# Kernel tuning notes

Measured on AMD Instinct MI355X. Metric: run time of the kernel, lower is better.

## Reference

```python
import jax, jax.numpy as jnp
import numpy as np

B, L, T = 64, 256, 800
NMEL, PRE, ARNN, DRNN, ENC, ATT, NF, K = 80, 256, 512, 512, 512, 128, 32, 31
ZP = 0.1  # zoneout prob (eval-mode expected-value interpolation)


def setup_inputs() -> dict:
    key = jax.random.key(0)
    ks = iter(jax.random.split(key, 32))
    def p(shape, s=0.05):
        return jax.random.normal(next(ks), shape, dtype=jnp.float32) * s
    inp = {
        'encoder_out': jax.random.normal(next(ks), (B, L, ENC), dtype=jnp.float32),
        'lengths': jax.random.randint(next(ks), (B,), L // 2, L + 1),
        'mels': jax.random.normal(next(ks), (B, T, NMEL), dtype=jnp.float32),
        # prenet: 3 bias-free linears with relu (eval: dropout off)
        'Wp1': p((PRE, NMEL)), 'Wp2': p((PRE, PRE)), 'Wp3': p((PRE, PRE)),
        # attention LSTMCell: input = prenet_dim + enc = 768
        'aWih': p((4 * ARNN, PRE + ENC)), 'aWhh': p((4 * ARNN, ARNN)),
        'abih': jnp.zeros((4 * ARNN,)), 'abhh': jnp.zeros((4 * ARNN,)),
        # decoder LSTMCell: input = att_rnn + enc = 1024
        'dWih': p((4 * DRNN, ARNN + ENC)), 'dWhh': p((4 * DRNN, DRNN)),
        'dbih': jnp.zeros((4 * DRNN,)), 'dbhh': jnp.zeros((4 * DRNN,)),
        # location-sensitive attention (all bias-free)
        'Wq': p((ATT, ARNN)), 'Wm': p((ATT, ENC)),
        'Wconv': p((NF, 2, K)), 'Wloc': p((ATT, NF)), 'v': p((1, ATT)),
        # output projection + gate
        'Wout': p((NMEL, DRNN + ENC)), 'bout': jnp.zeros((NMEL,)),
        'Wgate': p((1, DRNN + ENC)), 'bgate': jnp.zeros((1,)),
    }
    return inp


def _lstm(x, h, c, Wih, Whh, bih, bhh):
    g = x @ Wih.T + h @ Whh.T + (bih + bhh)
    i, f, gg, o = jnp.split(g, 4, axis=-1)
    c2 = jax.nn.sigmoid(f) * c + jax.nn.sigmoid(i) * jnp.tanh(gg)
    return jax.nn.sigmoid(o) * jnp.tanh(c2), c2


def _zoneout(new, old):
    return ZP * old + (1.0 - ZP) * new


def decoder_forward(encoder_out, lengths, mels, Wp1, Wp2, Wp3,
                    aWih, aWhh, abih, abhh, dWih, dWhh, dbih, dbhh,
                    Wq, Wm, Wconv, Wloc, v, Wout, bout, Wgate, bgate):
    b, l, _ = encoder_out.shape
    t = mels.shape[1]
    processed_memory = encoder_out @ Wm.T                       # (B,L,ATT)
    mask = jnp.arange(l)[None, :] >= lengths[:, None]           # True = padded
    # teacher forcing inputs: shift mels right by one zero frame
    dec_in = jnp.concatenate(
        [jnp.zeros((b, 1, NMEL), encoder_out.dtype), mels[:, :t - 1]], axis=1)
    xs = jnp.swapaxes(dec_in, 0, 1)                             # (T,B,NMEL)

    def step(carry, frame):
        ah, ac, dh, dc, ctx, aw, aws = carry
        x = jax.nn.relu(jax.nn.relu(jax.nn.relu(frame @ Wp1.T) @ Wp2.T) @ Wp3.T)
        ah2, ac2 = _lstm(jnp.concatenate([x, ctx], -1), ah, ac, aWih, aWhh, abih, abhh)
        ah2, ac2 = _zoneout(ah2, ah), _zoneout(ac2, ac)
        # location features: conv over (B,2,L)
        aw_cat = jnp.stack([aw, aws], axis=1)
        loc = jax.lax.conv_general_dilated(
            aw_cat, Wconv, window_strides=(1,), padding=[((K - 1) // 2,) * 2],
            dimension_numbers=('NCH', 'OIH', 'NCH'))                # (B,NF,L)
        ploc = jnp.swapaxes(loc, 1, 2) @ Wloc.T                      # (B,L,ATT)
        e = jnp.tanh(ah2[:, None, :] @ Wq.T + processed_memory + ploc)
        energies = jnp.squeeze(e @ v.T, -1)                          # (B,L)
        energies = jnp.where(mask, jnp.float32(-1e9), energies)
        w = jax.nn.softmax(energies, axis=-1)
        ctx2 = jnp.einsum('bl,ble->be', w, encoder_out)
        aws2 = aws + w
        dh2, dc2 = _lstm(jnp.concatenate([ah2, ctx2], -1), dh, dc, dWih, dWhh, dbih, dbhh)
        dh2, dc2 = _zoneout(dh2, dh), _zoneout(dc2, dc)
        dhc = jnp.concatenate([dh2, ctx2], axis=-1)
        mel = dhc @ Wout.T + bout
        gate = jnp.squeeze(dhc @ Wgate.T + bgate, -1)
        return (ah2, ac2, dh2, dc2, ctx2, w, aws2), (mel, gate, w)

    z = lambda *s: jnp.zeros(s, encoder_out.dtype)
    carry0 = (z(b, ARNN), z(b, ARNN), z(b, DRNN), z(b, DRNN), z(b, ENC), z(b, l), z(b, l))
    _, (mel_t, gate_t, align_t) = jax.lax.scan(step, carry0, xs)
    return (jnp.swapaxes(mel_t, 0, 1),      # (B,T,NMEL)
            jnp.swapaxes(gate_t, 0, 1),     # (B,T)
            jnp.swapaxes(align_t, 0, 1))    # (B,T,L)


def reference(encoder_out, lengths, mels, Wp1, Wp2, Wp3,
              aWih, aWhh, abih, abhh, dWih, dWhh, dbih, dbhh,
              Wq, Wm, Wconv, Wloc, v, Wout, bout, Wgate, bgate):
    return decoder_forward(encoder_out, lengths, mels, Wp1, Wp2, Wp3,
                           aWih, aWhh, abih, abhh, dWih, dWhh, dbih, dbhh,
                           Wq, Wm, Wconv, Wloc, v, Wout, bout, Wgate, bgate)
```

## Files before the change

kernel.cpp:

```cpp
#include <hip/hip_runtime.h>


#define DEV_INLINE __device__ __forceinline__

constexpr int TB = 800;

constexpr size_t PMT_O  = 0;
constexpr size_t WQT_O  = 2228224;
constexpr size_t LOCF_O = 2293760;
constexpr size_t Y1_O   = 2818048;
constexpr size_t Y2_O   = 2834432;
constexpr size_t XR_O   = 2850816;
constexpr size_t AH_O   = 2883584;
constexpr size_t AC_O   = 2949120;
constexpr size_t DH_O   = 3014656;
constexpr size_t DC_O   = 3080192;
constexpr size_t CTX_O  = 3145728;
constexpr size_t AW_O   = 3211264;
constexpr size_t AWS_O  = 3244032;
constexpr size_t BAR_O  = 3276800;
constexpr size_t ZERO_N = 991232;

constexpr size_t MEL_O  = 0;
constexpr size_t GATE_O = 4096000;
constexpr size_t ALG_O  = 4147200;

DEV_INLINE float sigf(float x)     { return 1.0f / (1.0f + __expf(-x)); }
DEV_INLINE float tanhfast(float x) { float e = __expf(2.0f * x); return 1.0f - 2.0f / (e + 1.0f); }

DEV_INLINE void stc(float* p, float v) {
  __hip_atomic_store(p, v, __ATOMIC_RELAXED, __HIP_MEMORY_SCOPE_AGENT);
}

struct Params {
  const float* enc; const int* len; const float* mels;
  const float* Wp1; const float* Wp2; const float* Wp3;
  const float* aWih; const float* aWhh; const float* abih; const float* abhh;
  const float* dWih; const float* dWhh; const float* dbih; const float* dbhh;
  const float* Wconv; const float* Wloc; const float* v;
  const float* Wout; const float* bout; const float* Wgate; const float* bgate;
  float* ws; float* out;
};

DEV_INLINE void gbar(unsigned* bar, int blk, bool iscap, unsigned e)
{
  __syncthreads();
  if (threadIdx.x == 0) {
    const unsigned g = (unsigned)blk >> 5;
    unsigned a = __hip_atomic_fetch_add(bar + g * 64, 1u, __ATOMIC_RELAXED, __HIP_MEMORY_SCOPE_AGENT);
    if (a == e * 32u - 1u)
      __hip_atomic_fetch_add(bar + 512, 1u, __ATOMIC_RELAXED, __HIP_MEMORY_SCOPE_AGENT);
    if (iscap) {
      while (__hip_atomic_load(bar + 512, __ATOMIC_RELAXED, __HIP_MEMORY_SCOPE_AGENT) < e * 8u)
        __builtin_amdgcn_s_sleep(1);
      __builtin_amdgcn_fence(__ATOMIC_ACQUIRE, "agent");
      const unsigned nc = __hip_atomic_load(bar + 2176, __ATOMIC_RELAXED, __HIP_MEMORY_SCOPE_AGENT);
      unsigned c = __hip_atomic_fetch_add(bar + 576, 1u, __ATOMIC_RELAXED, __HIP_MEMORY_SCOPE_AGENT);
      if (c == e * nc - 1u) {
#pragma unroll
        for (unsigned i = 0; i < 8; ++i)
          __hip_atomic_store(bar + 640 + i * 64, e, __ATOMIC_RELAXED, __HIP_MEMORY_SCOPE_AGENT);
      }
    }
    {
      const unsigned g2 = (unsigned)blk >> 5;
      while (__hip_atomic_load(bar + 640 + g2 * 64, __ATOMIC_RELAXED, __HIP_MEMORY_SCOPE_AGENT) < e)
        __builtin_amdgcn_s_sleep(4);
    }
  }
  __syncthreads();
  asm volatile("buffer_inv sc0\n\ts_waitcnt vmcnt(0)" ::: "memory");
}

DEV_INLINE void gseg16(float* __restrict__ acc,
                       const float* __restrict__ inT,
                       const float* __restrict__ W, const int ldw, const int wcol0,
                       const int u0, const int segk0, const int seglen,
                       const int ks, const int ke, const int lane)
{
  const int a0 = ks > segk0 ? ks : segk0;
  const int a1 = (ke < segk0 + seglen) ? ke : (segk0 + seglen);
  if (a0 >= a1) return;
  const float* __restrict__ ip = inT + (size_t)(a0 - segk0) * 64 + lane;
  const int n = a1 - a0;
  const float* wp[16];
#pragma unroll
  for (int j = 0; j < 16; ++j) {
    const int row = u0 + (j >> 2) + 512 * (j & 3);
    wp[j] = W + (size_t)row * ldw + (wcol0 + (a0 - segk0));
  }
  for (int k = 0; k < n; k += 4) {
    const float x0 = ip[(k + 0) * 64];
    const float x1 = ip[(k + 1) * 64];
    const float x2 = ip[(k + 2) * 64];
    const float x3 = ip[(k + 3) * 64];
#pragma unroll
    for (int j = 0; j < 16; ++j)
      acc[j] += x0 * wp[j][k] + x1 * wp[j][k + 1] + x2 * wp[j][k + 2] + x3 * wp[j][k + 3];
  }
}

template<int NO>
DEV_INLINE void gseg(float* __restrict__ acc,
                     const float* __restrict__ inT,
                     const float* __restrict__ W, const int ldw, const int wcol0,
                     const int* __restrict__ rows, const int segk0, const int seglen,
                     const int ks, const int ke, const int lane)
{
  const int a0 = ks > segk0 ? ks : segk0;
  const int a1 = (ke < segk0 + seglen) ? ke : (segk0 + seglen);
  if (a0 >= a1) return;
  const float* __restrict__ ip = inT + (size_t)(a0 - segk0) * 64 + lane;
  const int n = a1 - a0;
  const float* wp[NO];
#pragma unroll
  for (int j = 0; j < NO; ++j)
    wp[j] = W + (size_t)rows[j] * ldw + (wcol0 + (a0 - segk0));
  for (int k = 0; k < n; k += 4) {
    const float x0 = ip[(k + 0) * 64];
    const float x1 = ip[(k + 1) * 64];
    const float x2 = ip[(k + 2) * 64];
    const float x3 = ip[(k + 3) * 64];
#pragma unroll
    for (int j = 0; j < NO; ++j)
      acc[j] += x0 * wp[j][k] + x1 * wp[j][k + 1] + x2 * wp[j][k + 2] + x3 * wp[j][k + 3];
  }
}

__global__ __launch_bounds__(256) void init_kernel(const float* __restrict__ Wq,
                                                   float* __restrict__ ws)
{
  const int i = blockIdx.x * 256 + threadIdx.x;
  {
    const int k = i >> 7, a = i & 127;
    ws[WQT_O + i] = Wq[a * 512 + k];
  }
  for (size_t idx = i; idx < ZERO_N; idx += 65536)
    ws[LOCF_O + idx] = 0.0f;
}

__global__ __launch_bounds__(256) void prenet_kernel(const float* __restrict__ mels,
                                                     const float* __restrict__ Wp1,
                                                     const float* __restrict__ Wp2,
                                                     const float* __restrict__ Wp3,
                                                     float* __restrict__ xb)
{
  __shared__ float smem[16384];
  const int t = blockIdx.x;
  const int tid = threadIdx.x;
  const int lane = tid & 63;
  const int wv = __builtin_amdgcn_readfirstlane(tid >> 6);

  if (t == 0) {
    for (int i = tid; i < 5200; i += 256) smem[i] = 0.0f;
  } else {
    for (int i = tid; i < 5120; i += 256) {
      const int b = i / 80, k = i - b * 80;
      smem[k * 65 + b] = mels[((size_t)b * TB + (t - 1)) * 80 + k];
    }
  }
  __syncthreads();

  float va[8][8];
#pragma unroll
  for (int g = 0; g < 8; ++g) {
    const int u0 = wv * 64 + g * 8;
    float acc[8] = {};
    for (int k = 0; k < 80; ++k) {
      const float x = smem[k * 65 + lane];
#pragma unroll
      for (int j = 0; j < 8; ++j) acc[j] += x * Wp1[(u0 + j) * 80 + k];
    }
#pragma unroll
    for (int j = 0; j < 8; ++j) va[g][j] = fmaxf(acc[j], 0.0f);
  }
  __syncthreads();
#pragma unroll
  for (int g = 0; g < 8; ++g)
#pragma unroll
    for (int j = 0; j < 8; ++j) smem[(wv * 64 + g * 8 + j) * 64 + lane] = va[g][j];
  __syncthreads();

#pragma unroll
  for (int g = 0; g < 8; ++g) {
    const int u0 = wv * 64 + g * 8;
    float acc[8] = {};
    for (int k = 0; k < 256; ++k) {
      const float x = smem[k * 64 + lane];
#pragma unroll
      for (int j = 0; j < 8; ++j) acc[j] += x * Wp2[(u0 + j) * 256 + k];
    }
#pragma unroll
    for (int j = 0; j < 8; ++j) va[g][j] = fmaxf(acc[j], 0.0f);
  }
  __syncthreads();
#pragma unroll
  for (int g = 0; g < 8; ++g)
#pragma unroll
    for (int j = 0; j < 8; ++j) smem[(wv * 64 + g * 8 + j) * 64 + lane] = va[g][j];
  __syncthreads();

#pragma unroll
  for (int g = 0; g < 8; ++g) {
    const int u0 = wv * 64 + g * 8;
    float acc[8] = {};
    for (int k = 0; k < 256; ++k) {
      const float x = smem[k * 64 + lane];
#pragma unroll
      for (int j = 0; j < 8; ++j) acc[j] += x * Wp3[(u0 + j) * 256 + k];
    }
#pragma unroll
    for (int j = 0; j < 8; ++j)
      xb[((size_t)t * 256 + (u0 + j)) * 64 + lane] = fmaxf(acc[j], 0.0f);
  }
}

__global__ __launch_bounds__(256) void pm_kernel(const float* __restrict__ enc,
                                                 const float* __restrict__ Wm,
                                                 float* __restrict__ pmT)
{
  __shared__ float encL[64 * 129];
  const int b = blockIdx.x >> 2;
  const int l0 = (blockIdx.x & 3) * 64;
  const int tid = threadIdx.x;
  const int lane = tid & 63;
  const int wv = __builtin_amdgcn_readfirstlane(tid >> 6);

  float acc[4][8];
#pragma unroll
  for (int ai = 0; ai < 4; ++ai)
#pragma unroll
    for (int j = 0; j < 8; ++j) acc[ai][j] = 0.0f;

  for (int kc = 0; kc < 4; ++kc) {
    __syncthreads();
    for (int i = tid; i < 64 * 128; i += 256) {
      const int l = i >> 7, k = i & 127;
      encL[l * 129 + k] = enc[((size_t)b * 256 + l0 + l) * 512 + kc * 128 + k];
    }
    __syncthreads();
#pragma unroll
    for (int ai = 0; ai < 4; ++ai) {
      const int agrp = (ai * 4 + wv) * 8;
      for (int k = 0; k < 128; ++k) {
        const float x = encL[lane * 129 + k];
#pragma unroll
        for (int j = 0; j < 8; ++j)
          acc[ai][j] += x * Wm[(size_t)(agrp + j) * 512 + kc * 128 + k];
      }
    }
  }
#pragma unroll
  for (int ai = 0; ai < 4; ++ai) {
    const int agrp = (ai * 4 + wv) * 8;
#pragma unroll
    for (int j = 0; j < 8; ++j)
      pmT[((size_t)b * 128 + agrp + j) * 256 + l0 + lane] = acc[ai][j];
  }
}


DEV_INLINE void f_dgates4(int u0, int tid, int lane, int wv,
                          const float* __restrict__ ah, const float* __restrict__ dh,
                          float* __restrict__ gdL, const Params& p, float* sm)
{
  float acc[16] = {};
  const int ks = wv * 256, ke = ks + 256;
  gseg16(acc, ah, p.dWih, 1024, 0, u0, 0,   512, ks, ke, lane);
  gseg16(acc, dh, p.dWhh, 512,  0, u0, 512, 512, ks, ke, lane);
#pragma unroll
  for (int j = 0; j < 16; ++j) sm[(wv * 16 + j) * 64 + lane] = acc[j];
  __syncthreads();
  {
    const int m = tid & 63, uq = tid >> 6;
    const int u = u0 + uq;
#pragma unroll
    for (int q = 0; q < 4; ++q) {
      const int j = uq * 4 + q;
      gdL[j * 64 + m] = sm[j * 64 + m] + sm[(16 + j) * 64 + m] + sm[(32 + j) * 64 + m] + sm[(48 + j) * 64 + m]
                      + p.dbih[u + 512 * q] + p.dbhh[u + 512 * q];
    }
  }
  __syncthreads();
}

DEV_INLINE void f_dfin4(int u0, int tid, int lane, int wv,
                        const float* __restrict__ ctx, const float* __restrict__ gdL,
                        float* __restrict__ dh_o, float* __restrict__ dhL, float* __restrict__ dcL,
                        const Params& p, float* sm)
{
  float acc[16] = {};
  const int ks = wv * 128, ke = ks + 128;
  gseg16(acc, ctx, p.dWih, 1024, 512, u0, 0, 512, ks, ke, lane);
#pragma unroll
  for (int j = 0; j < 16; ++j) sm[(wv * 16 + j) * 64 + lane] = acc[j];
  __syncthreads();
  {
    const int m = tid & 63, uq = tid >> 6;
    const int u = u0 + uq;
    float g[4];
#pragma unroll
    for (int q = 0; q < 4; ++q) {
      const int j = uq * 4 + q;
      g[q] = sm[j * 64 + m] + sm[(16 + j) * 64 + m] + sm[(32 + j) * 64 + m] + sm[(48 + j) * 64 + m]
           + gdL[j * 64 + m];
    }
    const float ho = dhL[uq * 64 + m], co = dcL[uq * 64 + m];
    const float c2 = sigf(g[1]) * co + sigf(g[0]) * tanhfast(g[2]);
    const float h2 = sigf(g[3]) * tanhfast(c2);
    const float hn = 0.1f * ho + 0.9f * h2;
    const float cn = 0.1f * co + 0.9f * c2;
    stc(dh_o + (size_t)u * 64 + m, hn);
    dhL[uq * 64 + m] = hn;
    dcL[uq * 64 + m] = cn;
  }
  __syncthreads();
}

DEV_INLINE void f_alstm4(int u0, int tid, int lane, int wv,
                         const float* __restrict__ xt, const float* __restrict__ ctx,
                         const float* __restrict__ ahg,
                         float* __restrict__ ah_o, float* __restrict__ ahL, float* __restrict__ acL,
                         const Params& p, float* sm)
{
  float acc[16] = {};
  const int ks = wv * 320, ke = ks + 320;
  gseg16(acc, xt,  p.aWih, 768, 0,   u0, 0,   256, ks, ke, lane);
  gseg16(acc, ctx, p.aWih, 768, 256, u0, 256, 512, ks, ke, lane);
  gseg16(acc, ahg, p.aWhh, 512, 0,   u0, 768, 512, ks, ke, lane);
#pragma unroll
  for (int j = 0; j < 16; ++j) sm[(wv * 16 + j) * 64 + lane] = acc[j];
  __syncthreads();
  {
    const int m = tid & 63, uq = tid >> 6;
    const int u = u0 + uq;
    float g[4];
#pragma unroll
    for (int q = 0; q < 4; ++q) {
      const int j = uq * 4 + q;
      g[q] = sm[j * 64 + m] + sm[(16 + j) * 64 + m] + sm[(32 + j) * 64 + m] + sm[(48 + j) * 64 + m]
           + p.abih[u + 512 * q] + p.abhh[u + 512 * q];
    }
    const float ho = ahL[uq * 64 + m], co = acL[uq * 64 + m];
    const float c2 = sigf(g[1]) * co + sigf(g[0]) * tanhfast(g[2]);
    const float h2 = sigf(g[3]) * tanhfast(c2);
    const float hn = 0.1f * ho + 0.9f * h2;
    const float cn = 0.1f * co + 0.9f * c2;
    stc(ah_o + (size_t)u * 64 + m, hn);
    ahL[uq * 64 + m] = hn;
    acL[uq * 64 + m] = cn;
  }
  __syncthreads();
}

DEV_INLINE void f_mel(int c0, int tid, int lane, int wv, int tm1,
                      const float* __restrict__ dh, const float* __restrict__ ctx,
                      const Params& p, float* sm)
{
  int rows[4] = {c0, c0 + 1, c0 + 2, c0 + 3};
  float acc[4] = {};
  const int ks = wv * 256, ke = ks + 256;
  gseg<4>(acc, dh,  p.Wout, 1024, 0,   rows, 0,   512, ks, ke, lane);
  gseg<4>(acc, ctx, p.Wout, 1024, 512, rows, 512, 512, ks, ke, lane);
#pragma unroll
  for (int j = 0; j < 4; ++j) sm[(wv * 4 + j) * 64 + lane] = acc[j];
  __syncthreads();
  {
    const int m = tid & 63, c = tid >> 6;
    const float val = sm[c * 64 + m] + sm[(4 + c) * 64 + m] + sm[(8 + c) * 64 + m] + sm[(12 + c) * 64 + m]
                    + p.bout[c0 + c];
    stc(p.out + MEL_O + ((size_t)m * TB + tm1) * 80 + c0 + c, val);
  }
  __syncthreads();
}

DEV_INLINE void f_gate(int tid, int lane, int wv, int tm1,
                       const float* __restrict__ dh, const float* __restrict__ ctx,
                       const Params& p, float* sm)
{
  float acc[1] = {};
  int rows1[1] = {0};
  const int ks = wv * 256, ke = ks + 256;
  gseg<1>(acc, dh,  p.Wgate, 1024, 0,   rows1, 0,   512, ks, ke, lane);
  gseg<1>(acc, ctx, p.Wgate, 1024, 512, rows1, 512, 512, ks, ke, lane);
  sm[wv * 64 + lane] = acc[0];
  __syncthreads();
  if (tid < 64) {
    const float val = sm[tid] + sm[64 + tid] + sm[128 + tid] + sm[192 + tid] + p.bgate[0];
    stc(p.out + GATE_O + (size_t)tid * TB + tm1, val);
  }
  __syncthreads();
}

DEV_INLINE void f_conv(int b, int tid,
                       const float* __restrict__ aw, const float* __restrict__ aws,
                       float* __restrict__ locF, const Params& p, float* sm)
{
  float* awL  = sm;
  float* awsL = sm + 290;
  if (tid < 15) { awL[tid] = 0.0f; awsL[tid] = 0.0f; awL[271 + tid] = 0.0f; awsL[271 + tid] = 0.0f; }
  awL[15 + tid]  = aw[b * 256 + tid];
  awsL[15 + tid] = aws[b * 256 + tid];
  __syncthreads();
  float awv[31], awsv[31];
#pragma unroll
  for (int k = 0; k < 31; ++k) { awv[k] = awL[tid + k]; awsv[k] = awsL[tid + k]; }
  float* dst = locF + ((size_t)b * 256 + tid) * 32;
  for (int f = 0; f < 32; ++f) {
    const float* wc = p.Wconv + f * 62;
    float lf = 0.0f;
#pragma unroll
    for (int k = 0; k < 31; ++k) lf += awv[k] * wc[k] + awsv[k] * wc[31 + k];
    stc(dst + f, lf);
  }
  __syncthreads();
}

DEV_INLINE void f_energy(int b, int t, int tid, int lane, int wv,
                         const float* __restrict__ ah, const float* __restrict__ aws_p,
                         float* __restrict__ ctx_o, float* __restrict__ aw_o,
                         float* __restrict__ aws_o,
                         const float* __restrict__ pmT, const float* __restrict__ wqT,
                         const float* __restrict__ locF, const Params& p, float* sm)
{
  float* ahL = sm;
  float* qpL = sm + 512;
  float* qL  = sm + 768;
  float* red = sm + 896;
  float* wL  = sm + 912;
  ahL[tid]       = ah[(size_t)tid * 64 + b];
  ahL[tid + 256] = ah[(size_t)(tid + 256) * 64 + b];
  __syncthreads();
  {
    const int a = tid & 127, h = tid >> 7;
    float qp = 0.0f;
    const float* wq = wqT + (size_t)(h * 256) * 128 + a;
    const float* xv = ahL + h * 256;
    for (int k = 0; k < 256; k += 4)
      qp += wq[(k + 0) * 128] * xv[k + 0] + wq[(k + 1) * 128] * xv[k + 1]
          + wq[(k + 2) * 128] * xv[k + 2] + wq[(k + 3) * 128] * xv[k + 3];
    qpL[tid] = qp;
  }
  __syncthreads();
  if (tid < 128) qL[tid] = qpL[tid] + qpL[128 + tid];
  __syncthreads();

  float locv[32];
  {
    const float4* lf4 = (const float4*)(locF + ((size_t)b * 256 + tid) * 32);
#pragma unroll
    for (int i = 0; i < 8; ++i) {
      float4 x = lf4[i];
      locv[4*i] = x.x; locv[4*i+1] = x.y; locv[4*i+2] = x.z; locv[4*i+3] = x.w;
    }
  }
  float part = 0.0f;
  const float* pmp = pmT + (size_t)b * 32768 + tid;
#pragma unroll 2
  for (int a = 0; a < 128; ++a) {
    float s = qL[a] + pmp[(size_t)a * 256];
    const float* wl = p.Wloc + a * 32;
#pragma unroll
    for (int f = 0; f < 32; ++f) s += locv[f] * wl[f];
    part += p.v[a] * tanhfast(s);
  }
  if (tid >= p.len[b]) part = -1e9f;

  float mv = part;
  for (int mm = 32; mm >= 1; mm >>= 1) mv = fmaxf(mv, __shfl_xor(mv, mm, 64));
  if (lane == 0) red[wv] = mv;
  __syncthreads();
  const float mx = fmaxf(fmaxf(red[0], red[1]), fmaxf(red[2], red[3]));
  const float pex = __expf(part - mx);
  float ssum = pex;
  for (int mm = 32; mm >= 1; mm >>= 1) ssum += __shfl_xor(ssum, mm, 64);
  if (lane == 0) red[8 + wv] = ssum;
  __syncthreads();
  const float inv = 1.0f / (red[8] + red[9] + red[10] + red[11]);
  const float w = pex * inv;
  wL[tid] = w;
  stc(aw_o + b * 256 + tid, w);
  stc(aws_o + b * 256 + tid, aws_p[b * 256 + tid] + w);
  stc(p.out + ALG_O + ((size_t)b * TB + t) * 256 + tid, w);
  __syncthreads();

  float c0 = 0.0f, c1 = 0.0f;
  const float* ep = p.enc + (size_t)b * 256 * 512;
  for (int l = 0; l < 256; ++l) {
    const float wv_ = wL[l];
    c0 += wv_ * ep[(size_t)l * 512 + tid];
    c1 += wv_ * ep[(size_t)l * 512 + tid + 256];
  }
  stc(ctx_o + (size_t)tid * 64 + b, c0);
  stc(ctx_o + (size_t)(tid + 256) * 64 + b, c1);
  __syncthreads();
}

DEV_INLINE void f_pn1(int blkL, int frame, int lane, int wv,
                      const Params& p, float* __restrict__ y1)
{
  const int u0 = blkL * 32 + wv * 8;
  float acc[8] = {};
  const float* mp = p.mels + ((size_t)lane * TB + frame) * 80;
  for (int k = 0; k < 80; ++k) {
    const float x = mp[k];
#pragma unroll
    for (int j = 0; j < 8; ++j) acc[j] += x * p.Wp1[(u0 + j) * 80 + k];
  }
#pragma unroll
  for (int j = 0; j < 8; ++j) stc(y1 + (size_t)(u0 + j) * 64 + lane, fmaxf(acc[j], 0.0f));
}

DEV_INLINE void f_pnmid(int blkL, int lane, int wv,
                        const float* __restrict__ yin, const float* __restrict__ W,
                        float* __restrict__ yout)
{
  const int u0 = blkL * 32 + wv * 8;
  float acc[8] = {};
  for (int k = 0; k < 256; ++k) {
    const float x = yin[(size_t)k * 64 + lane];
#pragma unroll
    for (int j = 0; j < 8; ++j) acc[j] += x * W[(u0 + j) * 256 + k];
  }
#pragma unroll
  for (int j = 0; j < 8; ++j) stc(yout + (size_t)(u0 + j) * 64 + lane, fmaxf(acc[j], 0.0f));
}

__global__ __launch_bounds__(256) void persist_kernel(Params p)
{
  __shared__ float sm[4096];
  __shared__ float gdL[1024];
  __shared__ float s1L[256];
  __shared__ float s2L[256];
  __shared__ unsigned capflag;

  const int tid = threadIdx.x, blk = blockIdx.x;
  const int lane = tid & 63;
  const int wv = __builtin_amdgcn_readfirstlane(tid >> 6);
  const bool isX = blk < 128;
  const int yi = blk - 128;

  float* ws   = p.ws;
  float* pmT  = ws + PMT_O;
  float* wqT  = ws + WQT_O;
  float* locF = ws + LOCF_O;
  float* y1   = ws + Y1_O;
  float* y2   = ws + Y2_O;
  float* xr   = ws + XR_O;
  float* AH[2]  = {ws + AH_O,  ws + AH_O  + 32768};
  float* DH[2]  = {ws + DH_O,  ws + DH_O  + 32768};
  float* CTX[2] = {ws + CTX_O, ws + CTX_O + 32768};
  float* AW[2]  = {ws + AW_O,  ws + AW_O  + 16384};
  float* AWS[2] = {ws + AWS_O, ws + AWS_O + 16384};
  unsigned* bar = (unsigned*)(ws + BAR_O);

  s1L[tid] = 0.0f; s2L[tid] = 0.0f;
  if (tid == 0) {
    unsigned x;
    asm volatile("s_getreg_b32 %0, hwreg(HW_REG_XCC_ID)" : "=s"(x));
    unsigned prev = __hip_atomic_fetch_add(bar + 2048 + (x & 7), 1u,
                                           __ATOMIC_RELAXED, __HIP_MEMORY_SCOPE_AGENT);
    if (prev == 0)
      __hip_atomic_fetch_add(bar + 2176, 1u, __ATOMIC_RELAXED, __HIP_MEMORY_SCOPE_AGENT);
    capflag = (prev == 0) ? 1u : 0u;
  }
  __syncthreads();
  const bool iscap = (capflag != 0);
  unsigned e = 0;

  if (!isX && yi >= 85 && yi < 93) f_pn1(yi - 85, 1, lane, wv, p, y1);
  gbar(bar, blk, iscap, ++e);

  if (!isX) {
    f_alstm4(yi * 4, tid, lane, wv, xr, CTX[1], AH[1], AH[0], s1L, s2L, p, sm);
  } else if (blk < 8) {
    f_pnmid(blk, lane, wv, y1, p.Wp2, y2);
  }
  gbar(bar, blk, iscap, ++e);

  for (int t = 0; t < TB; ++t) {
    const int cur = t & 1, prv = cur ^ 1;
    if (isX) {
      f_dgates4(blk * 4, tid, lane, wv, AH[cur], DH[prv], gdL, p, sm);
    } else if (yi < 64) {
      f_energy(yi, t, tid, lane, wv, AH[cur], AWS[prv],
               CTX[cur], AW[cur], AWS[cur], pmT, wqT, locF, p, sm);
    } else if (yi < 84) {
      if (t > 0) f_mel((yi - 64) * 4, tid, lane, wv, t - 1, DH[prv], CTX[prv], p, sm);
    } else if (yi == 84) {
      if (t > 0) f_gate(tid, lane, wv, t - 1, DH[prv], CTX[prv], p, sm);
    } else if (yi < 93) {
      if (t <= 796) f_pn1(yi - 85, t + 2, lane, wv, p, y1);
    } else if (yi < 101) {
      if (t <= 797) f_pnmid(yi - 93, lane, wv, y2, p.Wp3, xr + (size_t)cur * 16384);
    }
    gbar(bar, blk, iscap, ++e);

    if (isX) {
      f_dfin4(blk * 4, tid, lane, wv, CTX[cur], gdL, DH[cur], s1L, s2L, p, sm);
      if (blk >= 64) {
        if (t < TB - 1) f_conv(blk - 64, tid, AW[cur], AWS[cur], locF, p, sm);
      } else if (blk < 8) {
        if (t <= 796) f_pnmid(blk, lane, wv, y1, p.Wp2, y2);
      }
    } else {
      if (t < TB - 1)
        f_alstm4(yi * 4, tid, lane, wv, xr + (size_t)prv * 16384, CTX[cur],
                 AH[cur], AH[prv], s1L, s2L, p, sm);
    }
    gbar(bar, blk, iscap, ++e);
  }
  if (!isX) {
    if (yi >= 64 && yi < 84)  f_mel((yi - 64) * 4, tid, lane, wv, TB - 1, DH[1], CTX[1], p, sm);
    else if (yi == 84)        f_gate(tid, lane, wv, TB - 1, DH[1], CTX[1], p, sm);
  }
}

extern "C" void kernel_launch(void* const* d_in, const int* in_sizes, int n_in,
                              void* d_out, int out_size, void* d_ws, size_t ws_size,
                              hipStream_t stream)
{
  (void)in_sizes; (void)n_in; (void)out_size; (void)ws_size;
  Params P;
  P.enc   = (const float*)d_in[0];
  P.len   = (const int*)  d_in[1];
  P.mels  = (const float*)d_in[2];
  P.Wp1   = (const float*)d_in[3];
  P.Wp2   = (const float*)d_in[4];
  P.Wp3   = (const float*)d_in[5];
  P.aWih  = (const float*)d_in[6];
  P.aWhh  = (const float*)d_in[7];
  P.abih  = (const float*)d_in[8];
  P.abhh  = (const float*)d_in[9];
  P.dWih  = (const float*)d_in[10];
  P.dWhh  = (const float*)d_in[11];
  P.dbih  = (const float*)d_in[12];
  P.dbhh  = (const float*)d_in[13];
  const float* Wq = (const float*)d_in[14];
  const float* Wm = (const float*)d_in[15];
  P.Wconv = (const float*)d_in[16];
  P.Wloc  = (const float*)d_in[17];
  P.v     = (const float*)d_in[18];
  P.Wout  = (const float*)d_in[19];
  P.bout  = (const float*)d_in[20];
  P.Wgate = (const float*)d_in[21];
  P.bgate = (const float*)d_in[22];
  P.ws  = (float*)d_ws;
  P.out = (float*)d_out;

  init_kernel<<<256, 256, 0, stream>>>(Wq, P.ws);
  pm_kernel<<<256, 256, 0, stream>>>(P.enc, Wm, P.ws + PMT_O);
  prenet_kernel<<<2, 256, 0, stream>>>(P.mels, P.Wp1, P.Wp2, P.Wp3, P.ws + XR_O);

  persist_kernel<<<256, 256, 0, stream>>>(P);
}
```

Before: 101.8 ms.

## Simplify grid barrier and replace cache invalidation with coherent loads

Replaces the per-XCD captain-based hierarchical barrier with a two-level counter tree whose last arriver releases all group flags. It also drops the full L2/L1 buffer_inv after each barrier. Instead, cross-block activation reads use relaxed agent-scope atomic loads, so weights stay cached. Wloc is staged into LDS for the energy blocks, and the context loop is unrolled. The risk is memory-ordering correctness: there is no acquire fence, and ordering now depends only on relaxed atomics.

```diff
diff --git a/kernel.cpp b/kernel.cpp
--- a/kernel.cpp
+++ b/kernel.cpp
@@ -12,9 +12,7 @@
 constexpr size_t Y2_O   = 2834432;
 constexpr size_t XR_O   = 2850816;
 constexpr size_t AH_O   = 2883584;
-constexpr size_t AC_O   = 2949120;
 constexpr size_t DH_O   = 3014656;
-constexpr size_t DC_O   = 3080192;
 constexpr size_t CTX_O  = 3145728;
 constexpr size_t AW_O   = 3211264;
 constexpr size_t AWS_O  = 3244032;
@@ -30,6 +28,9 @@
 
 DEV_INLINE void stc(float* p, float v) {
   __hip_atomic_store(p, v, __ATOMIC_RELAXED, __HIP_MEMORY_SCOPE_AGENT);
+}
+DEV_INLINE float ldc(const float* p) {
+  return __hip_atomic_load(p, __ATOMIC_RELAXED, __HIP_MEMORY_SCOPE_AGENT);
 }
 
 struct Params {
@@ -42,41 +43,31 @@
   float* ws; float* out;
 };
 
-DEV_INLINE void gbar(unsigned* bar, int blk, bool iscap, unsigned e)
+DEV_INLINE void gbar(unsigned* bar, int blk, unsigned e)
 {
   __syncthreads();
   if (threadIdx.x == 0) {
     const unsigned g = (unsigned)blk >> 5;
     unsigned a = __hip_atomic_fetch_add(bar + g * 64, 1u, __ATOMIC_RELAXED, __HIP_MEMORY_SCOPE_AGENT);
-    if (a == e * 32u - 1u)
-      __hip_atomic_fetch_add(bar + 512, 1u, __ATOMIC_RELAXED, __HIP_MEMORY_SCOPE_AGENT);
-    if (iscap) {
-      while (__hip_atomic_load(bar + 512, __ATOMIC_RELAXED, __HIP_MEMORY_SCOPE_AGENT) < e * 8u)
-        __builtin_amdgcn_s_sleep(1);
-      __builtin_amdgcn_fence(__ATOMIC_ACQUIRE, "agent");
-      const unsigned nc = __hip_atomic_load(bar + 2176, __ATOMIC_RELAXED, __HIP_MEMORY_SCOPE_AGENT);
-      unsigned c = __hip_atomic_fetch_add(bar + 576, 1u, __ATOMIC_RELAXED, __HIP_MEMORY_SCOPE_AGENT);
-      if (c == e * nc - 1u) {
+    if (a == e * 32u - 1u) {
+      unsigned r = __hip_atomic_fetch_add(bar + 512, 1u, __ATOMIC_RELAXED, __HIP_MEMORY_SCOPE_AGENT);
+      if (r == e * 8u - 1u) {
 #pragma unroll
         for (unsigned i = 0; i < 8; ++i)
           __hip_atomic_store(bar + 640 + i * 64, e, __ATOMIC_RELAXED, __HIP_MEMORY_SCOPE_AGENT);
       }
     }
-    {
-      const unsigned g2 = (unsigned)blk >> 5;
-      while (__hip_atomic_load(bar + 640 + g2 * 64, __ATOMIC_RELAXED, __HIP_MEMORY_SCOPE_AGENT) < e)
-        __builtin_amdgcn_s_sleep(4);
-    }
-  }
-  __syncthreads();
-  asm volatile("buffer_inv sc0\n\ts_waitcnt vmcnt(0)" ::: "memory");
-}
-
-DEV_INLINE void gseg16(float* __restrict__ acc,
-                       const float* __restrict__ inT,
-                       const float* __restrict__ W, const int ldw, const int wcol0,
-                       const int u0, const int segk0, const int seglen,
-                       const int ks, const int ke, const int lane)
+    while (__hip_atomic_load(bar + 640 + g * 64, __ATOMIC_RELAXED, __HIP_MEMORY_SCOPE_AGENT) < e)
+      __builtin_amdgcn_s_sleep(2);
+  }
+  __syncthreads();
+}
+
+DEV_INLINE void gseg16C(float* __restrict__ acc,
+                        const float* __restrict__ inT,
+                        const float* __restrict__ W, const int ldw, const int wcol0,
+                        const int u0, const int segk0, const int seglen,
+                        const int ks, const int ke, const int lane)
 {
   const int a0 = ks > segk0 ? ks : segk0;
   const int a1 = (ke < segk0 + seglen) ? ke : (segk0 + seglen);
@@ -90,10 +81,10 @@
     wp[j] = W + (size_t)row * ldw + (wcol0 + (a0 - segk0));
   }
   for (int k = 0; k < n; k += 4) {
-    const float x0 = ip[(k + 0) * 64];
-    const float x1 = ip[(k + 1) * 64];
-    const float x2 = ip[(k + 2) * 64];
-    const float x3 = ip[(k + 3) * 64];
+    const float x0 = ldc(ip + (k + 0) * 64);
+    const float x1 = ldc(ip + (k + 1) * 64);
+    const float x2 = ldc(ip + (k + 2) * 64);
+    const float x3 = ldc(ip + (k + 3) * 64);
 #pragma unroll
     for (int j = 0; j < 16; ++j)
       acc[j] += x0 * wp[j][k] + x1 * wp[j][k + 1] + x2 * wp[j][k + 2] + x3 * wp[j][k + 3];
@@ -101,11 +92,11 @@
 }
 
 template<int NO>
-DEV_INLINE void gseg(float* __restrict__ acc,
-                     const float* __restrict__ inT,
-                     const float* __restrict__ W, const int ldw, const int wcol0,
-                     const int* __restrict__ rows, const int segk0, const int seglen,
-                     const int ks, const int ke, const int lane)
+DEV_INLINE void gsegC(float* __restrict__ acc,
+                      const float* __restrict__ inT,
+                      const float* __restrict__ W, const int ldw, const int wcol0,
+                      const int* __restrict__ rows, const int segk0, const int seglen,
+                      const int ks, const int ke, const int lane)
 {
   const int a0 = ks > segk0 ? ks : segk0;
   const int a1 = (ke < segk0 + seglen) ? ke : (segk0 + seglen);
@@ -117,10 +108,10 @@
   for (int j = 0; j < NO; ++j)
     wp[j] = W + (size_t)rows[j] * ldw + (wcol0 + (a0 - segk0));
   for (int k = 0; k < n; k += 4) {
-    const float x0 = ip[(k + 0) * 64];
-    const float x1 = ip[(k + 1) * 64];
-    const float x2 = ip[(k + 2) * 64];
-    const float x3 = ip[(k + 3) * 64];
+    const float x0 = ldc(ip + (k + 0) * 64);
+    const float x1 = ldc(ip + (k + 1) * 64);
+    const float x2 = ldc(ip + (k + 2) * 64);
+    const float x3 = ldc(ip + (k + 3) * 64);
 #pragma unroll
     for (int j = 0; j < NO; ++j)
       acc[j] += x0 * wp[j][k] + x1 * wp[j][k + 1] + x2 * wp[j][k + 2] + x3 * wp[j][k + 3];
@@ -266,8 +257,8 @@
 {
   float acc[16] = {};
   const int ks = wv * 256, ke = ks + 256;
-  gseg16(acc, ah, p.dWih, 1024, 0, u0, 0,   512, ks, ke, lane);
-  gseg16(acc, dh, p.dWhh, 512,  0, u0, 512, 512, ks, ke, lane);
+  gseg16C(acc, ah, p.dWih, 1024, 0, u0, 0,   512, ks, ke, lane);
+  gseg16C(acc, dh, p.dWhh, 512,  0, u0, 512, 512, ks, ke, lane);
 #pragma unroll
   for (int j = 0; j < 16; ++j) sm[(wv * 16 + j) * 64 + lane] = acc[j];
   __syncthreads();
@@ -291,7 +282,7 @@
 {
   float acc[16] = {};
   const int ks = wv * 128, ke = ks + 128;
-  gseg16(acc, ctx, p.dWih, 1024, 512, u0, 0, 512, ks, ke, lane);
+  gseg16C(acc, ctx, p.dWih, 1024, 512, u0, 0, 512, ks, ke, lane);
 #pragma unroll
   for (int j = 0; j < 16; ++j) sm[(wv * 16 + j) * 64 + lane] = acc[j];
   __syncthreads();
@@ -325,9 +316,9 @@
 {
   float acc[16] = {};
   const int ks = wv * 320, ke = ks + 320;
-  gseg16(acc, xt,  p.aWih, 768, 0,   u0, 0,   256, ks, ke, lane);
-  gseg16(acc, ctx, p.aWih, 768, 256, u0, 256, 512, ks, ke, lane);
-  gseg16(acc, ahg, p.aWhh, 512, 0,   u0, 768, 512, ks, ke, lane);
+  gseg16C(acc, xt,  p.aWih, 768, 0,   u0, 0,   256, ks, ke, lane);
+  gseg16C(acc, ctx, p.aWih, 768, 256, u0, 256, 512, ks, ke, lane);
+  gseg16C(acc, ahg, p.aWhh, 512, 0,   u0, 768, 512, ks, ke, lane);
 #pragma unroll
   for (int j = 0; j < 16; ++j) sm[(wv * 16 + j) * 64 + lane] = acc[j];
   __syncthreads();
@@ -360,8 +351,8 @@
   int rows[4] = {c0, c0 + 1, c0 + 2, c0 + 3};
   float acc[4] = {};
   const int ks = wv * 256, ke = ks + 256;
-  gseg<4>(acc, dh,  p.Wout, 1024, 0,   rows, 0,   512, ks, ke, lane);
-  gseg<4>(acc, ctx, p.Wout, 1024, 512, rows, 512, 512, ks, ke, lane);
+  gsegC<4>(acc, dh,  p.Wout, 1024, 0,   rows, 0,   512, ks, ke, lane);
+  gsegC<4>(acc, ctx, p.Wout, 1024, 512, rows, 512, 512, ks, ke, lane);
 #pragma unroll
   for (int j = 0; j < 4; ++j) sm[(wv * 4 + j) * 64 + lane] = acc[j];
   __syncthreads();
@@ -381,8 +372,8 @@
   float acc[1] = {};
   int rows1[1] = {0};
   const int ks = wv * 256, ke = ks + 256;
-  gseg<1>(acc, dh,  p.Wgate, 1024, 0,   rows1, 0,   512, ks, ke, lane);
-  gseg<1>(acc, ctx, p.Wgate, 1024, 512, rows1, 512, 512, ks, ke, lane);
+  gsegC<1>(acc, dh,  p.Wgate, 1024, 0,   rows1, 0,   512, ks, ke, lane);
+  gsegC<1>(acc, ctx, p.Wgate, 1024, 512, rows1, 512, 512, ks, ke, lane);
   sm[wv * 64 + lane] = acc[0];
   __syncthreads();
   if (tid < 64) {
@@ -399,8 +390,8 @@
   float* awL  = sm;
   float* awsL = sm + 290;
   if (tid < 15) { awL[tid] = 0.0f; awsL[tid] = 0.0f; awL[271 + tid] = 0.0f; awsL[271 + tid] = 0.0f; }
-  awL[15 + tid]  = aw[b * 256 + tid];
-  awsL[15 + tid] = aws[b * 256 + tid];
+  awL[15 + tid]  = ldc(aw + b * 256 + tid);
+  awsL[15 + tid] = ldc(aws + b * 256 + tid);
   __syncthreads();
   float awv[31], awsv[31];
 #pragma unroll
@@ -421,15 +412,16 @@
                          float* __restrict__ ctx_o, float* __restrict__ aw_o,
                          float* __restrict__ aws_o,
                          const float* __restrict__ pmT, const float* __restrict__ wqT,
-                         const float* __restrict__ locF, const Params& p, float* sm)
+                         const float* __restrict__ locF, const float* __restrict__ wlocL,
+                         const Params& p, float* sm)
 {
   float* ahL = sm;
   float* qpL = sm + 512;
   float* qL  = sm + 768;
   float* red = sm + 896;
   float* wL  = sm + 912;
-  ahL[tid]       = ah[(size_t)tid * 64 + b];
-  ahL[tid + 256] = ah[(size_t)(tid + 256) * 64 + b];
+  ahL[tid]       = ldc(ah + (size_t)tid * 64 + b);
+  ahL[tid + 256] = ldc(ah + (size_t)(tid + 256) * 64 + b);
   __syncthreads();
   {
     const int a = tid & 127, h = tid >> 7;
@@ -447,19 +439,16 @@
 
   float locv[32];
   {
-    const float4* lf4 = (const float4*)(locF + ((size_t)b * 256 + tid) * 32);
-#pragma unroll
-    for (int i = 0; i < 8; ++i) {
-      float4 x = lf4[i];
-      locv[4*i] = x.x; locv[4*i+1] = x.y; locv[4*i+2] = x.z; locv[4*i+3] = x.w;
-    }
+    const float* lf = locF + ((size_t)b * 256 + tid) * 32;
+#pragma unroll
+    for (int i = 0; i < 32; ++i) locv[i] = ldc(lf + i);
   }
   float part = 0.0f;
   const float* pmp = pmT + (size_t)b * 32768 + tid;
 #pragma unroll 2
   for (int a = 0; a < 128; ++a) {
     float s = qL[a] + pmp[(size_t)a * 256];
-    const float* wl = p.Wloc + a * 32;
+    const float* wl = wlocL + a * 32;
 #pragma unroll
     for (int f = 0; f < 32; ++f) s += locv[f] * wl[f];
     part += p.v[a] * tanhfast(s);
@@ -480,12 +469,13 @@
   const float w = pex * inv;
   wL[tid] = w;
   stc(aw_o + b * 256 + tid, w);
-  stc(aws_o + b * 256 + tid, aws_p[b * 256 + tid] + w);
+  stc(aws_o + b * 256 + tid, ldc(aws_p + b * 256 + tid) + w);
   stc(p.out + ALG_O + ((size_t)b * TB + t) * 256 + tid, w);
   __syncthreads();
 
   float c0 = 0.0f, c1 = 0.0f;
   const float* ep = p.enc + (size_t)b * 256 * 512;
+#pragma unroll 4
   for (int l = 0; l < 256; ++l) {
     const float wv_ = wL[l];
     c0 += wv_ * ep[(size_t)l * 512 + tid];
@@ -518,7 +508,7 @@
   const int u0 = blkL * 32 + wv * 8;
   float acc[8] = {};
   for (int k = 0; k < 256; ++k) {
-    const float x = yin[(size_t)k * 64 + lane];
+    const float x = ldc(yin + (size_t)k * 64 + lane);
 #pragma unroll
     for (int j = 0; j < 8; ++j) acc[j] += x * W[(u0 + j) * 256 + k];
   }
@@ -532,7 +522,7 @@
   __shared__ float gdL[1024];
   __shared__ float s1L[256];
   __shared__ float s2L[256];
-  __shared__ unsigned capflag;
+  __shared__ float wlocL[4096];
 
   const int tid = threadIdx.x, blk = blockIdx.x;
   const int lane = tid & 63;
@@ -554,29 +544,22 @@
   float* AWS[2] = {ws + AWS_O, ws + AWS_O + 16384};
   unsigned* bar = (unsigned*)(ws + BAR_O);
 
+  if (!isX && yi < 64)
+    for (int i = tid; i < 4096; i += 256) wlocL[i] = p.Wloc[i];
+
   s1L[tid] = 0.0f; s2L[tid] = 0.0f;
-  if (tid == 0) {
-    unsigned x;
-    asm volatile("s_getreg_b32 %0, hwreg(HW_REG_XCC_ID)" : "=s"(x));
-    unsigned prev = __hip_atomic_fetch_add(bar + 2048 + (x & 7), 1u,
-                                           __ATOMIC_RELAXED, __HIP_MEMORY_SCOPE_AGENT);
-    if (prev == 0)
-      __hip_atomic_fetch_add(bar + 2176, 1u, __ATOMIC_RELAXED, __HIP_MEMORY_SCOPE_AGENT);
-    capflag = (prev == 0) ? 1u : 0u;
-  }
-  __syncthreads();
-  const bool iscap = (capflag != 0);
+  __syncthreads();
   unsigned e = 0;
 
   if (!isX && yi >= 85 && yi < 93) f_pn1(yi - 85, 1, lane, wv, p, y1);
-  gbar(bar, blk, iscap, ++e);
+  gbar(bar, blk, ++e);
 
   if (!isX) {
     f_alstm4(yi * 4, tid, lane, wv, xr, CTX[1], AH[1], AH[0], s1L, s2L, p, sm);
   } else if (blk < 8) {
     f_pnmid(blk, lane, wv, y1, p.Wp2, y2);
   }
-  gbar(bar, blk, iscap, ++e);
+  gbar(bar, blk, ++e);
 
   for (int t = 0; t < TB; ++t) {
     const int cur = t & 1, prv = cur ^ 1;
@@ -584,7 +567,7 @@
       f_dgates4(blk * 4, tid, lane, wv, AH[cur], DH[prv], gdL, p, sm);
     } else if (yi < 64) {
       f_energy(yi, t, tid, lane, wv, AH[cur], AWS[prv],
-               CTX[cur], AW[cur], AWS[cur], pmT, wqT, locF, p, sm);
+               CTX[cur], AW[cur], AWS[cur], pmT, wqT, locF, wlocL, p, sm);
     } else if (yi < 84) {
       if (t > 0) f_mel((yi - 64) * 4, tid, lane, wv, t - 1, DH[prv], CTX[prv], p, sm);
     } else if (yi == 84) {
@@ -594,7 +577,7 @@
     } else if (yi < 101) {
       if (t <= 797) f_pnmid(yi - 93, lane, wv, y2, p.Wp3, xr + (size_t)cur * 16384);
     }
-    gbar(bar, blk, iscap, ++e);
+    gbar(bar, blk, ++e);
 
     if (isX) {
       f_dfin4(blk * 4, tid, lane, wv, CTX[cur], gdL, DH[cur], s1L, s2L, p, sm);
@@ -608,7 +591,7 @@
         f_alstm4(yi * 4, tid, lane, wv, xr + (size_t)prv * 16384, CTX[cur],
                  AH[cur], AH[prv], s1L, s2L, p, sm);
     }
-    gbar(bar, blk, iscap, ++e);
+    gbar(bar, blk, ++e);
   }
   if (!isX) {
     if (yi >= 64 && yi < 84)  f_mel((yi - 64) * 4, tid, lane, wv, TB - 1, DH[1], CTX[1], p, sm);
```

After: 105.6 ms. 3.7% more time.
